# Performance work log

Measured on AMD Instinct MI355X. Metric: run time of the kernel, lower is better.

## Reference

```python
import jax, jax.numpy as jnp
import numpy as np

MARGIN = 0.2
NEG_SENTINEL = -1e30


def setup_inputs() -> dict:
    key = jax.random.key(0)
    k1, k2 = jax.random.split(key)
    batch_reprs = jax.random.normal(k1, (4096, 128), dtype=jnp.float32)
    batch_labels = jax.random.randint(k2, (4096,), 0, 512, dtype=jnp.int64 if jax.config.jax_enable_x64 else jnp.int32)
    return {"batch_reprs": batch_reprs, "batch_labels": batch_labels}


def _loss(batch_reprs, batch_labels):
    # class match matrix (self-similarity kept, as in original)
    match = (batch_labels[:, None] == batch_labels[None, :]).astype(batch_reprs.dtype)  # [B,B]

    # pairwise euclidean distance (squared=False), sim = -dist
    sq = jnp.sum(batch_reprs * batch_reprs, axis=1)
    d2 = jnp.maximum(sq[:, None] + sq[None, :] - 2.0 * (batch_reprs @ batch_reprs.T), 0.0)
    zero = (d2 == 0.0).astype(batch_reprs.dtype)
    dist = jnp.sqrt(d2 + zero * 1e-16) * (1.0 - zero)
    sim_hat = -dist + (1.0 - match) * MARGIN  # use_margin=True

    # rank positions via double argsort (descending)
    order = jnp.argsort(-sim_hat, axis=1)
    rank = jnp.argsort(order, axis=1).astype(sim_hat.dtype) + 1.0  # [B,B], 1-based ranks

    k = jnp.sum(match, axis=1, keepdims=True)                      # n_pos per row, [B,1]
    fp = (match < 1.0) & (rank <= k)                               # false positives
    fp_num = jnp.sum(fp, axis=1, keepdims=True).astype(sim_hat.dtype)
    fn = (match > 0.0) & (rank > k)                                # false negatives

    n = sim_hat.shape[1]
    # per-row top-(fp_num) false negatives by sim_hat, vectorized via masked sort
    fn_scores = jnp.where(fn, sim_hat, NEG_SENTINEL)
    idx = jnp.argsort(-fn_scores, axis=1)
    fn_sorted = jnp.take_along_axis(sim_hat, idx, axis=1)
    fn_ranks = jnp.take_along_axis(rank, idx, axis=1)
    fn_mask_sorted = jnp.take_along_axis(fn, idx, axis=1)
    sel = (jnp.arange(n)[None, :] < fp_num) & fn_mask_sorted       # top fp_num entries

    # weighted margins (rows with fp_num==0 contribute 0 automatically)
    fp_term = jnp.sum(jnp.where(fp, sim_hat * (0.5 + (k - rank + 1.0) / k * 0.5), 0.0))
    fn_term = jnp.sum(jnp.where(sel, fn_sorted * (0.5 + (fn_ranks - k) / (n - k) * 0.5), 0.0))
    return fp_term - fn_term


def reference(batch_reprs, batch_labels):
    return _loss(batch_reprs, batch_labels)
```

## Files before the change

kernel.cpp:

```cpp
#include <hip/hip_runtime.h>
#include <cstdint>
#include <cstddef>

#define B 4096
#define D 128
#define MARGIN_F 0.2f
#define CW 256
#define ROWS 16
#define SSTR 4104

typedef short bf16x8 __attribute__((ext_vector_type(8)));
typedef float f32x4 __attribute__((ext_vector_type(4)));
typedef uint32_t u32x4 __attribute__((ext_vector_type(4)));

__device__ __forceinline__ uint32_t xform_key(float f) {
    uint32_t u = __float_as_uint(f);
    return u ^ (uint32_t)((((int32_t)u) >> 31) | 0x80000000);
}
__device__ __forceinline__ float unxform16(uint32_t k16) {
    uint32_t u = k16 << 16;
    u = (u & 0x80000000u) ? (u ^ 0x80000000u) : ~u;
    return __uint_as_float(u);
}
__device__ __forceinline__ unsigned short f2bf(float f) {
    uint32_t u = __float_as_uint(f);
    return (unsigned short)((u + 0x7FFFu + ((u >> 16) & 1u)) >> 16);
}

__global__ __launch_bounds__(256) void prep_kernel(const float* __restrict__ R,
                                                   float* __restrict__ sq,
                                                   unsigned short* __restrict__ Rb,
                                                   float* __restrict__ out) {
    if (blockIdx.x == 0 && threadIdx.x == 0) out[0] = 0.0f;
    int wave = threadIdx.x >> 6;
    int lane = threadIdx.x & 63;
    int row  = blockIdx.x * 4 + wave;
    const float2* R2 = (const float2*)R + (size_t)row * (D / 2);
    float2 v = R2[lane];
    ushort2 o; o.x = f2bf(v.x); o.y = f2bf(v.y);
    *(ushort2*)(Rb + (size_t)row * D + lane * 2) = o;
    float s = v.x * v.x + v.y * v.y;
#pragma unroll
    for (int off = 32; off > 0; off >>= 1) s += __shfl_down(s, off);
    if (lane == 0) sq[row] = s;
}

__global__ __launch_bounds__(512) void fused_loss(const unsigned short* __restrict__ Rb,
                                                  const float* __restrict__ sq,
                                                  const int* __restrict__ labels,
                                                  float* __restrict__ out) {
    __shared__ unsigned short S[ROWS * SSTR];
    __shared__ uint32_t cand_c[ROWS][CW];

    const int tid  = threadIdx.x;
    const int wid  = tid >> 6, lane = tid & 63;
    const int q    = lane >> 4, t = lane & 15;
    const int r0   = blockIdx.x * ROWS;

    {
        uint32_t* cz = &cand_c[0][0];
#pragma unroll
        for (int c = 0; c < (ROWS * CW) / 512; ++c)
            cz[tid + c * 512] = 0u;
    }

    bf16x8 af[4];
    const unsigned short* baseA = Rb + (size_t)(r0 + t) * D + q * 8;
#pragma unroll
    for (int kq = 0; kq < 4; ++kq)
        af[kq] = *(const bf16x8*)(baseA + kq * 32);

    float sqa[4]; int la[4];
#pragma unroll
    for (int rr = 0; rr < 4; ++rr) {
        sqa[rr] = sq[r0 + q * 4 + rr];
        la[rr]  = labels[r0 + q * 4 + rr];
    }

    for (int i = 0; i < 32; ++i) {
        const int jt  = wid * 32 + i;
        const int col = jt * 16 + t;
        const unsigned short* baseB = Rb + (size_t)col * D + q * 8;
        bf16x8 bfr[4];
#pragma unroll
        for (int kq = 0; kq < 4; ++kq)
            bfr[kq] = *(const bf16x8*)(baseB + kq * 32);
        f32x4 acc = (f32x4)0.0f;
#pragma unroll
        for (int kq = 0; kq < 4; ++kq)
            acc = __builtin_amdgcn_mfma_f32_16x16x32_bf16(af[kq], bfr[kq], acc, 0, 0, 0);

        const float sqc = sq[col];
        const int   lc  = labels[col];
#pragma unroll
        for (int rr = 0; rr < 4; ++rr) {
            float g  = acc[rr];
            float d2 = fmaxf(sqa[rr] + sqc - 2.0f * g, 0.0f);
            float dist = (d2 > 0.0f) ? sqrtf(d2) : 0.0f;
            float s = -dist + ((la[rr] == lc) ? 0.0f : MARGIN_F);
            uint32_t key = xform_key(s);
            S[(q * 4 + rr) * SSTR + col] = (unsigned short)((key + 0x8000u) >> 16);
        }
    }
    __syncthreads();

    float facc = 0.0f;
    const int4* lv = (const int4*)labels;

    for (int rr2 = 0; rr2 < 2; ++rr2) {
        const int row  = wid * 2 + rr2;
        const int grow = r0 + row;
        const int li   = labels[grow];

        uint64_t mbits = 0;
        uint32_t t1 = 0, t2 = 0;
        int total = 0;

        {
            u32x4 kv[8];
#pragma unroll
            for (int qq = 0; qq < 8; ++qq)
                kv[qq] = *(u32x4*)(&S[row * SSTR + (qq * 64 + lane) * 8]);

            uint32_t t1a[8], t2a[8];
#pragma unroll
            for (int qq = 0; qq < 8; ++qq) {
                const int lb = (qq * 64 + lane) * 2;
                int4 la4 = lv[lb], lc4 = lv[lb + 1];
                uint32_t u[8] = {kv[qq].x & 0xFFFFu, kv[qq].x >> 16,
                                 kv[qq].y & 0xFFFFu, kv[qq].y >> 16,
                                 kv[qq].z & 0xFFFFu, kv[qq].z >> 16,
                                 kv[qq].w & 0xFFFFu, kv[qq].w >> 16};
                uint32_t l1 = 0, l2 = 0;
#pragma unroll
                for (int c = 0; c < 8; ++c) {
                    uint32_t mn = min(l1, u[c]);
                    l1 = max(l1, u[c]);
                    l2 = max(l2, mn);
                }
                t1a[qq] = l1; t2a[qq] = l2;
                mbits |= (uint64_t)(la4.x == li) << (qq * 8 + 0);
                mbits |= (uint64_t)(la4.y == li) << (qq * 8 + 1);
                mbits |= (uint64_t)(la4.z == li) << (qq * 8 + 2);
                mbits |= (uint64_t)(la4.w == li) << (qq * 8 + 3);
                mbits |= (uint64_t)(lc4.x == li) << (qq * 8 + 4);
                mbits |= (uint64_t)(lc4.y == li) << (qq * 8 + 5);
                mbits |= (uint64_t)(lc4.z == li) << (qq * 8 + 6);
                mbits |= (uint64_t)(lc4.w == li) << (qq * 8 + 7);
            }
#pragma unroll
            for (int qq = 0; qq < 8; ++qq) {
                uint32_t mn = min(t1, t1a[qq]);
                t1 = max(t1, t1a[qq]);
                t2 = max(t2, mn);
                mn = min(t1, t2a[qq]);
                t1 = max(t1, t2a[qq]);
                t2 = max(t2, mn);
            }

            int kloc = __popcll(mbits);
#pragma unroll
            for (int off = 32; off > 0; off >>= 1) kloc += __shfl_xor(kloc, off);
            const int k0 = kloc;

            const int kneed = min(k0, 128);
            uint32_t T = 0;
#pragma unroll
            for (int b = 15; b >= 0; --b) {
                uint32_t g = T | (1u << b);
                int c = __popcll(__ballot(t1 >= g)) + __popcll(__ballot(t2 >= g));
                if (c >= kneed) T = g;
            }

            uint64_t wmask = 0;
#pragma unroll
            for (int qq = 0; qq < 8; ++qq) {
                uint32_t u[8] = {kv[qq].x & 0xFFFFu, kv[qq].x >> 16,
                                 kv[qq].y & 0xFFFFu, kv[qq].y >> 16,
                                 kv[qq].z & 0xFFFFu, kv[qq].z >> 16,
                                 kv[qq].w & 0xFFFFu, kv[qq].w >> 16};
#pragma unroll
                for (int c = 0; c < 8; ++c) {
                    int e = qq * 8 + c;
                    uint32_t m = (uint32_t)((mbits >> e) & 1);
                    wmask |= (uint64_t)((u[c] >= T) | m) << e;
                }
            }
            int cw = __popcll(wmask);
            int inc = cw;
#pragma unroll
            for (int off = 1; off < 64; off <<= 1) {
                int v = __shfl_up(inc, off);
                if (lane >= off) inc += v;
            }
            int mybase = inc - cw;
            total = __shfl(inc, 63);

#pragma unroll
            for (int qq = 0; qq < 8; ++qq) {
                uint32_t sub = (uint32_t)((wmask >> (qq * 8)) & 0xFFu);
                uint32_t u[8] = {kv[qq].x & 0xFFFFu, kv[qq].x >> 16,
                                 kv[qq].y & 0xFFFFu, kv[qq].y >> 16,
                                 kv[qq].z & 0xFFFFu, kv[qq].z >> 16,
                                 kv[qq].w & 0xFFFFu, kv[qq].w >> 16};
                int jb = (qq * 64 + lane) * 8;
#pragma unroll
                for (int c = 0; c < 8; ++c) {
                    if (sub & (1u << c)) {
                        if (mybase < CW) {
                            uint32_t m = (uint32_t)((mbits >> (qq * 8 + c)) & 1);
                            cand_c[row][mybase] =
                                (u[c] << 12) | (uint32_t)(4095 - (jb + c)) | (m << 31);
                        }
                        ++mybase;
                    }
                }
            }

            t1 = T;
            t2 = (uint32_t)k0;
        }

        const uint32_t T = t1;
        const int k = (int)t2;
        const float kf = (float)k;
        const uint32_t combT = T << 12;
        const int ncand = min(total, CW);

        __builtin_amdgcn_s_waitcnt(0);

        uint32_t cr0 = cand_c[row][lane];
        uint32_t cr1 = cand_c[row][lane + 64];
        uint32_t cr2 = cand_c[row][lane + 128];
        uint32_t cr3 = cand_c[row][lane + 192];
        uint32_t mycomb[4] = {cr0 & 0x7FFFFFFFu, cr1 & 0x7FFFFFFFu,
                              cr2 & 0x7FFFFFFFu, cr3 & 0x7FFFFFFFu};
        int mym[4]  = {(int)(cr0 >> 31), (int)(cr1 >> 31),
                       (int)(cr2 >> 31), (int)(cr3 >> 31)};
        int myok[4] = {lane < ncand, lane + 64 < ncand,
                       lane + 128 < ncand, lane + 192 < ncand};
        int myc[4]  = {0, 0, 0, 0};

        const int npad = (ncand + 7) & ~7;
        for (int c0i = 0; c0i < npad; c0i += 8) {
            u32x4 a = *(const u32x4*)&cand_c[row][c0i];
            u32x4 b = *(const u32x4*)&cand_c[row][c0i + 4];
            uint32_t vv[8] = {a.x, a.y, a.z, a.w, b.x, b.y, b.z, b.w};
#pragma unroll
            for (int e = 0; e < 8; ++e) {
                uint32_t vm = vv[e] & 0x7FFFFFFFu;
#pragma unroll
                for (int j = 0; j < 4; ++j)
                    myc[j] += (vm > mycomb[j]) ? 1 : 0;
            }
        }

#pragma unroll
        for (int j = 0; j < 4; ++j) {
            if (myok[j] && mycomb[j] >= combT) {
                int rank = 1 + myc[j];
                float v = unxform16(mycomb[j] >> 12);
                if (!mym[j] && rank <= k)
                    facc += v * (0.5f + ((kf - (float)rank + 1.0f) / kf) * 0.5f);
                else if (mym[j] && rank > k)
                    facc -= v * (0.5f + (((float)rank - kf) / (float)(B - k)) * 0.5f);
            }
        }

        uint32_t p0 = 0xFFFFFFFFu, p1 = 0xFFFFFFFFu, p2 = 0xFFFFFFFFu, p3 = 0xFFFFFFFFu;

        auto flush4 = [&](int npv) {
            int c0 = 0, c1 = 0, c2 = 0, c3 = 0;
#pragma unroll
            for (int qq = 0; qq < 8; ++qq) {
                u32x4 kq = *(const u32x4*)(&S[row * SSTR + (qq * 64 + lane) * 8]);
                uint32_t u[8] = {kq.x & 0xFFFFu, kq.x >> 16,
                                 kq.y & 0xFFFFu, kq.y >> 16,
                                 kq.z & 0xFFFFu, kq.z >> 16,
                                 kq.w & 0xFFFFu, kq.w >> 16};
                int jb = (qq * 64 + lane) * 8;
#pragma unroll
                for (int cc = 0; cc < 8; ++cc) {
                    uint32_t ce = (u[cc] << 12) | (uint32_t)(4095 - (jb + cc));
                    c0 += (ce > p0) ? 1 : 0;  c1 += (ce > p1) ? 1 : 0;
                    c2 += (ce > p2) ? 1 : 0;  c3 += (ce > p3) ? 1 : 0;
                }
            }
#pragma unroll
            for (int off = 32; off > 0; off >>= 1) {
                c0 += __shfl_xor(c0, off); c1 += __shfl_xor(c1, off);
                c2 += __shfl_xor(c2, off); c3 += __shfl_xor(c3, off);
            }
            if (lane == 0) {
                if (npv > 0) facc -= unxform16(p0 >> 12) * (0.5f + (((float)(1 + c0) - kf) / (float)(B - k)) * 0.5f);
                if (npv > 1) facc -= unxform16(p1 >> 12) * (0.5f + (((float)(1 + c1) - kf) / (float)(B - k)) * 0.5f);
                if (npv > 2) facc -= unxform16(p2 >> 12) * (0.5f + (((float)(1 + c2) - kf) / (float)(B - k)) * 0.5f);
                if (npv > 3) facc -= unxform16(p3 >> 12) * (0.5f + (((float)(1 + c3) - kf) / (float)(B - k)) * 0.5f);
            }
            p0 = p1 = p2 = p3 = 0xFFFFFFFFu;
        };

        int np = 0;
#pragma unroll
        for (int j = 0; j < 4; ++j) {
            uint64_t mg = __ballot(myok[j] && mym[j] && (mycomb[j] < combT));
            while (mg) {
                int src = __ffsll((unsigned long long)mg) - 1;
                mg &= mg - 1;
                uint32_t pc;
                if (j == 0)      pc = __shfl(mycomb[0], src);
                else if (j == 1) pc = __shfl(mycomb[1], src);
                else if (j == 2) pc = __shfl(mycomb[2], src);
                else             pc = __shfl(mycomb[3], src);
                switch (np) {
                    case 0: p0 = pc; break; case 1: p1 = pc; break;
                    case 2: p2 = pc; break; default: p3 = pc; break;
                }
                ++np;
                if (np == 4) { flush4(4); np = 0; }
            }
        }
        if (np > 0) flush4(np);
    }

#pragma unroll
    for (int off = 32; off > 0; off >>= 1) facc += __shfl_xor(facc, off);
    if (lane == 0) atomicAdd(out, facc);
}

extern "C" void kernel_launch(void* const* d_in, const int* in_sizes, int n_in,
                              void* d_out, int out_size, void* d_ws, size_t ws_size,
                              hipStream_t stream) {
    const float* R      = (const float*)d_in[0];
    const int*   labels = (const int*)d_in[1];
    float* out = (float*)d_out;

    float*          sq = (float*)d_ws;
    unsigned short* Rb = (unsigned short*)((char*)d_ws + 16 * 1024);

    hipLaunchKernelGGL(prep_kernel, dim3(B / 4), dim3(256), 0, stream, R, sq, Rb, out);
    hipLaunchKernelGGL(fused_loss, dim3(B / ROWS), dim3(512), 0, stream,
                       Rb, sq, labels, out);
}
```

Before: 133.0 us.

## Software-pipeline B-fragment loads and re-read LDS rows to cut register pressure

The MFMA tile loop now prefetches the next column's bf16 fragments, squared norm and label while computing the current tile, a one-step software pipeline. The per-row selection phase no longer keeps all eight 128-bit key vectors in registers. It re-reads them from LDS in each pass, and several loops are forced not to unroll. Together these aim to lower VGPR usage and so raise occupancy, and to hide global load latency. The cost is extra LDS reads and more loop overhead.

```diff
diff --git a/kernel.cpp b/kernel.cpp
--- a/kernel.cpp
+++ b/kernel.cpp
@@ -77,29 +77,51 @@
         la[rr]  = labels[r0 + q * 4 + rr];
     }
 
-    for (int i = 0; i < 32; ++i) {
-        const int jt  = wid * 32 + i;
-        const int col = jt * 16 + t;
-        const unsigned short* baseB = Rb + (size_t)col * D + q * 8;
+    {
+        const int jt0 = wid * 32;
+        int col = jt0 * 16 + t;
         bf16x8 bfr[4];
-#pragma unroll
-        for (int kq = 0; kq < 4; ++kq)
-            bfr[kq] = *(const bf16x8*)(baseB + kq * 32);
-        f32x4 acc = (f32x4)0.0f;
-#pragma unroll
-        for (int kq = 0; kq < 4; ++kq)
-            acc = __builtin_amdgcn_mfma_f32_16x16x32_bf16(af[kq], bfr[kq], acc, 0, 0, 0);
-
-        const float sqc = sq[col];
-        const int   lc  = labels[col];
-#pragma unroll
-        for (int rr = 0; rr < 4; ++rr) {
-            float g  = acc[rr];
-            float d2 = fmaxf(sqa[rr] + sqc - 2.0f * g, 0.0f);
-            float dist = (d2 > 0.0f) ? sqrtf(d2) : 0.0f;
-            float s = -dist + ((la[rr] == lc) ? 0.0f : MARGIN_F);
-            uint32_t key = xform_key(s);
-            S[(q * 4 + rr) * SSTR + col] = (unsigned short)((key + 0x8000u) >> 16);
+        {
+            const unsigned short* baseB = Rb + (size_t)col * D + q * 8;
+#pragma unroll
+            for (int kq = 0; kq < 4; ++kq)
+                bfr[kq] = *(const bf16x8*)(baseB + kq * 32);
+        }
+        float sqc = sq[col];
+        int   lc  = labels[col];
+
+#pragma unroll 1
+        for (int i = 0; i < 32; ++i) {
+            const int jn   = (i < 31) ? (jt0 + i + 1) : (jt0 + 31);
+            const int coln = jn * 16 + t;
+            bf16x8 bnx[4];
+            {
+                const unsigned short* baseB = Rb + (size_t)coln * D + q * 8;
+#pragma unroll
+                for (int kq = 0; kq < 4; ++kq)
+                    bnx[kq] = *(const bf16x8*)(baseB + kq * 32);
+            }
+            const float sqn = sq[coln];
+            const int   lcn = labels[coln];
+
+            f32x4 acc = (f32x4)0.0f;
+#pragma unroll
+            for (int kq = 0; kq < 4; ++kq)
+                acc = __builtin_amdgcn_mfma_f32_16x16x32_bf16(af[kq], bfr[kq], acc, 0, 0, 0);
+
+#pragma unroll
+            for (int rr = 0; rr < 4; ++rr) {
+                float g  = acc[rr];
+                float d2 = fmaxf(sqa[rr] + sqc - 2.0f * g, 0.0f);
+                float dist = (d2 > 0.0f) ? sqrtf(d2) : 0.0f;
+                float s = -dist + ((la[rr] == lc) ? 0.0f : MARGIN_F);
+                uint32_t key = xform_key(s);
+                S[(q * 4 + rr) * SSTR + col] = (unsigned short)((key + 0x8000u) >> 16);
+            }
+
+#pragma unroll
+            for (int kq = 0; kq < 4; ++kq) bfr[kq] = bnx[kq];
+            sqc = sqn; lc = lcn; col = coln;
         }
     }
     __syncthreads();
@@ -107,124 +129,112 @@
     float facc = 0.0f;
     const int4* lv = (const int4*)labels;
 
+#pragma unroll 1
     for (int rr2 = 0; rr2 < 2; ++rr2) {
         const int row  = wid * 2 + rr2;
-        const int grow = r0 + row;
-        const int li   = labels[grow];
+        const int li   = labels[r0 + row];
+        const unsigned short* Srow = &S[row * SSTR];
 
         uint64_t mbits = 0;
         uint32_t t1 = 0, t2 = 0;
-        int total = 0;
-
-        {
-            u32x4 kv[8];
-#pragma unroll
-            for (int qq = 0; qq < 8; ++qq)
-                kv[qq] = *(u32x4*)(&S[row * SSTR + (qq * 64 + lane) * 8]);
-
-            uint32_t t1a[8], t2a[8];
-#pragma unroll
-            for (int qq = 0; qq < 8; ++qq) {
-                const int lb = (qq * 64 + lane) * 2;
-                int4 la4 = lv[lb], lc4 = lv[lb + 1];
-                uint32_t u[8] = {kv[qq].x & 0xFFFFu, kv[qq].x >> 16,
-                                 kv[qq].y & 0xFFFFu, kv[qq].y >> 16,
-                                 kv[qq].z & 0xFFFFu, kv[qq].z >> 16,
-                                 kv[qq].w & 0xFFFFu, kv[qq].w >> 16};
-                uint32_t l1 = 0, l2 = 0;
-#pragma unroll
-                for (int c = 0; c < 8; ++c) {
-                    uint32_t mn = min(l1, u[c]);
-                    l1 = max(l1, u[c]);
-                    l2 = max(l2, mn);
+
+#pragma unroll 1
+        for (int qq = 0; qq < 8; ++qq) {
+            u32x4 kq = *(const u32x4*)(Srow + (qq * 64 + lane) * 8);
+            const int lb = (qq * 64 + lane) * 2;
+            int4 la4 = lv[lb], lc4 = lv[lb + 1];
+            uint32_t u[8] = {kq.x & 0xFFFFu, kq.x >> 16,
+                             kq.y & 0xFFFFu, kq.y >> 16,
+                             kq.z & 0xFFFFu, kq.z >> 16,
+                             kq.w & 0xFFFFu, kq.w >> 16};
+            uint32_t l1 = 0, l2 = 0;
+#pragma unroll
+            for (int c = 0; c < 8; ++c) {
+                uint32_t mn = min(l1, u[c]);
+                l1 = max(l1, u[c]);
+                l2 = max(l2, mn);
+            }
+            uint32_t mn = min(t1, l1);
+            t1 = max(t1, l1);
+            t2 = max(t2, mn);
+            mn = min(t1, l2);
+            t1 = max(t1, l2);
+            t2 = max(t2, mn);
+            uint32_t mloc = (uint32_t)(la4.x == li)
+                          | ((uint32_t)(la4.y == li) << 1)
+                          | ((uint32_t)(la4.z == li) << 2)
+                          | ((uint32_t)(la4.w == li) << 3)
+                          | ((uint32_t)(lc4.x == li) << 4)
+                          | ((uint32_t)(lc4.y == li) << 5)
+                          | ((uint32_t)(lc4.z == li) << 6)
+                          | ((uint32_t)(lc4.w == li) << 7);
+            mbits |= (uint64_t)mloc << (qq * 8);
+        }
+
+        int kloc = __popcll(mbits);
+#pragma unroll
+        for (int off = 32; off > 0; off >>= 1) kloc += __shfl_xor(kloc, off);
+        const int k = kloc;
+        const float kf = (float)k;
+
+        const int kneed = min(k, 128);
+        uint32_t T = 0;
+#pragma unroll 1
+        for (int b = 15; b >= 0; --b) {
+            uint32_t g = T | (1u << b);
+            int c = __popcll(__ballot(t1 >= g)) + __popcll(__ballot(t2 >= g));
+            if (c >= kneed) T = g;
+        }
+        const uint32_t combT = T << 12;
+
+        uint64_t wmask = 0;
+#pragma unroll 1
+        for (int qq = 0; qq < 8; ++qq) {
+            u32x4 kq = *(const u32x4*)(Srow + (qq * 64 + lane) * 8);
+            uint32_t u[8] = {kq.x & 0xFFFFu, kq.x >> 16,
+                             kq.y & 0xFFFFu, kq.y >> 16,
+                             kq.z & 0xFFFFu, kq.z >> 16,
+                             kq.w & 0xFFFFu, kq.w >> 16};
+            uint32_t msub = (uint32_t)((mbits >> (qq * 8)) & 0xFFu);
+            uint32_t wsub = 0;
+#pragma unroll
+            for (int c = 0; c < 8; ++c)
+                wsub |= ((uint32_t)(u[c] >= T) | ((msub >> c) & 1u)) << c;
+            wmask |= (uint64_t)wsub << (qq * 8);
+        }
+
+        int cw = __popcll(wmask);
+        int inc = cw;
+#pragma unroll
+        for (int off = 1; off < 64; off <<= 1) {
+            int v = __shfl_up(inc, off);
+            if (lane >= off) inc += v;
+        }
+        int mybase = inc - cw;
+        const int total = __shfl(inc, 63);
+
+#pragma unroll 1
+        for (int qq = 0; qq < 8; ++qq) {
+            u32x4 kq = *(const u32x4*)(Srow + (qq * 64 + lane) * 8);
+            uint32_t u[8] = {kq.x & 0xFFFFu, kq.x >> 16,
+                             kq.y & 0xFFFFu, kq.y >> 16,
+                             kq.z & 0xFFFFu, kq.z >> 16,
+                             kq.w & 0xFFFFu, kq.w >> 16};
+            uint32_t sub  = (uint32_t)((wmask >> (qq * 8)) & 0xFFu);
+            uint32_t msub = (uint32_t)((mbits >> (qq * 8)) & 0xFFu);
+            int jb = (qq * 64 + lane) * 8;
+#pragma unroll
+            for (int c = 0; c < 8; ++c) {
+                if (sub & (1u << c)) {
+                    if (mybase < CW) {
+                        uint32_t m = (msub >> c) & 1u;
+                        cand_c[row][mybase] =
+                            (u[c] << 12) | (uint32_t)(4095 - (jb + c)) | (m << 31);
+                    }
+                    ++mybase;
                 }
-                t1a[qq] = l1; t2a[qq] = l2;
-                mbits |= (uint64_t)(la4.x == li) << (qq * 8 + 0);
-                mbits |= (uint64_t)(la4.y == li) << (qq * 8 + 1);
-                mbits |= (uint64_t)(la4.z == li) << (qq * 8 + 2);
-                mbits |= (uint64_t)(la4.w == li) << (qq * 8 + 3);
-                mbits |= (uint64_t)(lc4.x == li) << (qq * 8 + 4);
-                mbits |= (uint64_t)(lc4.y == li) << (qq * 8 + 5);
-                mbits |= (uint64_t)(lc4.z == li) << (qq * 8 + 6);
-                mbits |= (uint64_t)(lc4.w == li) << (qq * 8 + 7);
-            }
-#pragma unroll
-            for (int qq = 0; qq < 8; ++qq) {
-                uint32_t mn = min(t1, t1a[qq]);
-                t1 = max(t1, t1a[qq]);
-                t2 = max(t2, mn);
-                mn = min(t1, t2a[qq]);
-                t1 = max(t1, t2a[qq]);
-                t2 = max(t2, mn);
-            }
-
-            int kloc = __popcll(mbits);
-#pragma unroll
-            for (int off = 32; off > 0; off >>= 1) kloc += __shfl_xor(kloc, off);
-            const int k0 = kloc;
-
-            const int kneed = min(k0, 128);
-            uint32_t T = 0;
-#pragma unroll
-            for (int b = 15; b >= 0; --b) {
-                uint32_t g = T | (1u << b);
-                int c = __popcll(__ballot(t1 >= g)) + __popcll(__ballot(t2 >= g));
-                if (c >= kneed) T = g;
-            }
-
-            uint64_t wmask = 0;
-#pragma unroll
-            for (int qq = 0; qq < 8; ++qq) {
-                uint32_t u[8] = {kv[qq].x & 0xFFFFu, kv[qq].x >> 16,
-                                 kv[qq].y & 0xFFFFu, kv[qq].y >> 16,
-                                 kv[qq].z & 0xFFFFu, kv[qq].z >> 16,
-                                 kv[qq].w & 0xFFFFu, kv[qq].w >> 16};
-#pragma unroll
-                for (int c = 0; c < 8; ++c) {
-                    int e = qq * 8 + c;
-                    uint32_t m = (uint32_t)((mbits >> e) & 1);
-                    wmask |= (uint64_t)((u[c] >= T) | m) << e;
-                }
-            }
-            int cw = __popcll(wmask);
-            int inc = cw;
-#pragma unroll
-            for (int off = 1; off < 64; off <<= 1) {
-                int v = __shfl_up(inc, off);
-                if (lane >= off) inc += v;
-            }
-            int mybase = inc - cw;
-            total = __shfl(inc, 63);
-
-#pragma unroll
-            for (int qq = 0; qq < 8; ++qq) {
-                uint32_t sub = (uint32_t)((wmask >> (qq * 8)) & 0xFFu);
-                uint32_t u[8] = {kv[qq].x & 0xFFFFu, kv[qq].x >> 16,
-                                 kv[qq].y & 0xFFFFu, kv[qq].y >> 16,
-                                 kv[qq].z & 0xFFFFu, kv[qq].z >> 16,
-                                 kv[qq].w & 0xFFFFu, kv[qq].w >> 16};
-                int jb = (qq * 64 + lane) * 8;
-#pragma unroll
-                for (int c = 0; c < 8; ++c) {
-                    if (sub & (1u << c)) {
-                        if (mybase < CW) {
-                            uint32_t m = (uint32_t)((mbits >> (qq * 8 + c)) & 1);
-                            cand_c[row][mybase] =
-                                (u[c] << 12) | (uint32_t)(4095 - (jb + c)) | (m << 31);
-                        }
-                        ++mybase;
-                    }
-                }
-            }
-
-            t1 = T;
-            t2 = (uint32_t)k0;
-        }
-
-        const uint32_t T = t1;
-        const int k = (int)t2;
-        const float kf = (float)k;
-        const uint32_t combT = T << 12;
+            }
+        }
         const int ncand = min(total, CW);
 
         __builtin_amdgcn_s_waitcnt(0);
@@ -242,6 +252,7 @@
         int myc[4]  = {0, 0, 0, 0};
 
         const int npad = (ncand + 7) & ~7;
+#pragma unroll 1
         for (int c0i = 0; c0i < npad; c0i += 8) {
             u32x4 a = *(const u32x4*)&cand_c[row][c0i];
             u32x4 b = *(const u32x4*)&cand_c[row][c0i + 4];
@@ -271,9 +282,9 @@
 
         auto flush4 = [&](int npv) {
             int c0 = 0, c1 = 0, c2 = 0, c3 = 0;
-#pragma unroll
+#pragma unroll 1
             for (int qq = 0; qq < 8; ++qq) {
-                u32x4 kq = *(const u32x4*)(&S[row * SSTR + (qq * 64 + lane) * 8]);
+                u32x4 kq = *(const u32x4*)(Srow + (qq * 64 + lane) * 8);
                 uint32_t u[8] = {kq.x & 0xFFFFu, kq.x >> 16,
                                  kq.y & 0xFFFFu, kq.y >> 16,
                                  kq.z & 0xFFFFu, kq.z >> 16,
```

After: 145.5 us. 9.5% more time.
